# Kernel tuning notes

Measured on AMD Instinct MI355X. Metric: run time of the kernel, lower is better.

Reference implementation:

```python
import jax, jax.numpy as jnp
import numpy as np

TEMPERATURE = 8.0  # sqrt(d_k=64)

def setup_inputs() -> dict:
    key = jax.random.key(0)
    ks = jax.random.split(key, 6)
    shape = (16, 2048, 64)  # [batch*heads, seq_len, d_k]
    names = ["q_real", "k_real", "v_real", "q_phase", "k_phase", "v_phase"]
    return {n: jax.random.normal(k, shape, dtype=jnp.float32) for n, k in zip(names, ks)}

def reference(q_real, k_real, v_real, q_phase, k_phase, v_phase):
    # Complex QK^T scores: (q_r + i q_p)(k_r + i k_p)^H-style split used by the module
    attn_real = jnp.einsum('bqd,bkd->bqk', q_real, k_real) - jnp.einsum('bqd,bkd->bqk', q_phase, k_phase)
    attn_phase = jnp.einsum('bqd,bkd->bqk', q_real, k_phase) + jnp.einsum('bqd,bkd->bqk', q_phase, k_real)
    # continue_complex=True path, mask=None, dropout in eval (p effectively 0)
    attn_real = jax.nn.softmax(attn_real / TEMPERATURE, axis=2)
    attn_phase = jax.nn.softmax(attn_phase / TEMPERATURE, axis=2)
    output_real = jnp.einsum('bqk,bkd->bqd', attn_real, v_real) - jnp.einsum('bqk,bkd->bqd', attn_phase, v_phase)
    output_phase = jnp.einsum('bqk,bkd->bqd', attn_real, v_phase) + jnp.einsum('bqk,bkd->bqd', attn_phase, v_real)
    return output_real, output_phase, attn_real
```

## Files before the change

kernel.cpp:

```cpp
#include <hip/hip_runtime.h>
#include <hip/hip_bf16.h>
#include <stdint.h>

#define BATCH 16
#define SEQ   2048
#define DK    64
#define BQ    (BATCH * SEQ)
#define MAT   ((size_t)BQ * DK)

typedef float  f32x4  __attribute__((ext_vector_type(4)));
typedef __bf16 bf16x8 __attribute__((ext_vector_type(8)));
typedef unsigned short u16x8 __attribute__((ext_vector_type(8)));
typedef unsigned short u16x4 __attribute__((ext_vector_type(4)));

#define MFMA16(a, b, c) __builtin_amdgcn_mfma_f32_16x16x32_bf16((a), (b), (c), 0, 0, 0)

#define TILEU 16384

__device__ __forceinline__ unsigned short bfbits(float f) {
  return __builtin_bit_cast(unsigned short, __float2bfloat16(f));
}

__device__ __forceinline__ void cvt_store(unsigned short* dst, f32x4 a, f32x4 c) {
  u16x8 v;
  v[0] = bfbits(a[0]); v[1] = bfbits(a[1]); v[2] = bfbits(a[2]); v[3] = bfbits(a[3]);
  v[4] = bfbits(c[0]); v[5] = bfbits(c[1]); v[6] = bfbits(c[2]); v[7] = bfbits(c[3]);
  *(u16x8*)dst = v;
}

__device__ __forceinline__ void gload16(const unsigned short* g, unsigned short* l) {
  __builtin_amdgcn_global_load_lds(
      (const __attribute__((address_space(1))) void*)g,
      (__attribute__((address_space(3))) void*)l, 16, 0, 0);
}

__global__ __launch_bounds__(256)
void ck_prep(const float* __restrict__ kr, const float* __restrict__ kp,
             const float* __restrict__ vr, const float* __restrict__ vp,
             const float* __restrict__ qr, const float* __restrict__ qp,
             unsigned short* __restrict__ kv, unsigned short* __restrict__ qb)
{
  __shared__ __align__(16) unsigned short VL[8192];
  const int tid = threadIdx.x;

  if (blockIdx.x >= BATCH * 32) {
    const size_t i8 = ((size_t)(blockIdx.x - BATCH * 32) * 256 + tid) * 8;
    const float* src = (i8 < MAT) ? qr : qp;
    const size_t off = (i8 < MAT) ? i8 : i8 - MAT;
    f32x4 a = *(const f32x4*)(src + off);
    f32x4 c = *(const f32x4*)(src + off + 4);
    cvt_store(qb + i8, a, c);
    return;
  }

  const int b = blockIdx.x >> 5, tile = blockIdx.x & 31;
  unsigned short* blk = kv + (size_t)(b * 32 + tile) * TILEU;
  const size_t go = ((size_t)b * SEQ + tile * 64) * DK;

  {
    const int row = tid >> 2, cp = tid & 3, sw = row & 7;
    const int c0 = cp * 2, c1 = cp * 2 + 1;
    const float* gr = kr + go + (size_t)row * DK + cp * 16;
    f32x4 r0 = ((const f32x4*)gr)[0], r1 = ((const f32x4*)gr)[1];
    f32x4 r2 = ((const f32x4*)gr)[2], r3 = ((const f32x4*)gr)[3];
    const float* gp = kp + go + (size_t)row * DK + cp * 16;
    f32x4 p0 = ((const f32x4*)gp)[0], p1 = ((const f32x4*)gp)[1];
    f32x4 p2 = ((const f32x4*)gp)[2], p3 = ((const f32x4*)gp)[3];
    cvt_store(blk + row * 64 + (c0 ^ sw) * 8, r0, r1);
    cvt_store(blk + row * 64 + (c1 ^ sw) * 8, r2, r3);
    cvt_store(blk + 4096 + row * 64 + (c0 ^ sw) * 8, p0, p1);
    cvt_store(blk + 4096 + row * 64 + (c1 ^ sw) * 8, p2, p3);
  }
  {
    const int key = tid & 15, d0 = (tid >> 4) * 4;
    #pragma unroll
    for (int pass = 0; pass < 4; ++pass) {
      const int kk = pass * 16 + key;
      f32x4 a = *(const f32x4*)(vr + go + (size_t)kk * DK + d0);
      f32x4 c = *(const f32x4*)(vp + go + (size_t)kk * DK + d0);
      const int kc = kk >> 3, kl = kk & 7;
      #pragma unroll
      for (int j = 0; j < 4; ++j) {
        const int d = d0 + j;
        VL[d * 64 + (kc ^ (d & 7)) * 8 + kl]        = bfbits(a[j]);
        VL[4096 + d * 64 + (kc ^ (d & 7)) * 8 + kl] = bfbits(c[j]);
      }
    }
  }
  __syncthreads();
  #pragma unroll
  for (int it = 0; it < 4; ++it)
    *(u16x8*)(blk + 8192 + it * 2048 + tid * 8) = *(const u16x8*)(VL + it * 2048 + tid * 8);
}

__global__ __launch_bounds__(256, 4)
void ck_sums(const unsigned short* __restrict__ qb,
             const unsigned short* __restrict__ kv, float* __restrict__ wsums)
{
  __shared__ __align__(16) unsigned short KT[2][8192];

  const int tid  = threadIdx.x;
  const int wq   = tid >> 6, lane = tid & 63;
  const int lrow = lane & 15, lgrp = lane >> 4;

  const int hw = blockIdx.x;
  const int logical = (hw & 7) * 256 + (hw >> 3);
  const int b = logical >> 7, qtile = (logical >> 2) & 31, slice = logical & 3;

  const int qrow = qtile * 64 + wq * 16 + lrow;
  const size_t qoff = ((size_t)b * SEQ + qrow) * DK;
  bf16x8 aQ0 = __builtin_bit_cast(bf16x8, *(const u16x8*)(qb + qoff + lgrp * 8));
  bf16x8 aQ1 = __builtin_bit_cast(bf16x8, *(const u16x8*)(qb + qoff + 32 + lgrp * 8));
  bf16x8 aQ2 = __builtin_bit_cast(bf16x8, *(const u16x8*)(qb + MAT + qoff + lgrp * 8));
  bf16x8 aQ3 = __builtin_bit_cast(bf16x8, *(const u16x8*)(qb + MAT + qoff + 32 + lgrp * 8));

  auto issue = [&](int tile, int buf) {
    const unsigned short* src = kv + (size_t)(b * 32 + tile) * TILEU;
    #pragma unroll
    for (int c = 0; c < 4; ++c) {
      const int ch = wq * 4 + c;
      gload16(src + ch * 512 + lane * 8, &KT[buf][ch * 512]);
    }
  };

  float lsR[4] = {0.f, 0.f, 0.f, 0.f};
  float lsP[4] = {0.f, 0.f, 0.f, 0.f};

  issue(slice * 8 + 0, 0);
  issue(slice * 8 + 1, 1);
  int cur = 0;
  for (int i = 0; i < 8; ++i) {
    if (i < 7) { asm volatile("s_waitcnt vmcnt(4)" ::: "memory"); }
    else       { asm volatile("s_waitcnt vmcnt(0)" ::: "memory"); }
    __builtin_amdgcn_sched_barrier(0);
    __syncthreads();

    const unsigned short* KB = KT[cur];
    #pragma unroll
    for (int t = 0; t < 4; ++t) {
      const int key16 = t * 16 + lrow;
      const int swk = lrow & 7;
      bf16x8 b0 = __builtin_bit_cast(bf16x8, *(const u16x8*)&KB[key16 * 64 + ((lgrp    ) ^ swk) * 8]);
      bf16x8 b1 = __builtin_bit_cast(bf16x8, *(const u16x8*)&KB[key16 * 64 + ((lgrp + 4) ^ swk) * 8]);
      bf16x8 b2 = __builtin_bit_cast(bf16x8, *(const u16x8*)&KB[4096 + key16 * 64 + ((lgrp    ) ^ swk) * 8]);
      bf16x8 b3 = __builtin_bit_cast(bf16x8, *(const u16x8*)&KB[4096 + key16 * 64 + ((lgrp + 4) ^ swk) * 8]);
      f32x4 t1 = {}, t2 = {}, sp = {};
      t1 = MFMA16(aQ0, b0, t1); t1 = MFMA16(aQ1, b1, t1);
      t2 = MFMA16(aQ2, b2, t2); t2 = MFMA16(aQ3, b3, t2);
      sp = MFMA16(aQ0, b2, sp); sp = MFMA16(aQ1, b3, sp);
      sp = MFMA16(aQ2, b0, sp); sp = MFMA16(aQ3, b1, sp);
      #pragma unroll
      for (int r = 0; r < 4; ++r) {
        lsR[r] += __expf((t1[r] - t2[r]) * 0.125f);
        lsP[r] += __expf(sp[r] * 0.125f);
      }
    }
    __syncthreads();
    if (i + 2 < 8) issue(slice * 8 + i + 2, cur);
    cur ^= 1;
  }

  #pragma unroll
  for (int r = 0; r < 4; ++r) {
    float sR = lsR[r], sP = lsP[r];
    #pragma unroll
    for (int m = 1; m < 16; m <<= 1) {
      sR += __shfl_xor(sR, m, 64);
      sP += __shfl_xor(sP, m, 64);
    }
    if (lrow == 0) {
      const size_t row = (size_t)b * SEQ + qtile * 64 + wq * 16 + lgrp * 4 + r;
      wsums[(size_t)(slice * 2 + 0) * BQ + row] = sR;
      wsums[(size_t)(slice * 2 + 1) * BQ + row] = sP;
    }
  }
}

__global__ __launch_bounds__(256, 2)
void ck_main(const unsigned short* __restrict__ qb,
             const unsigned short* __restrict__ kv,
             const float* __restrict__ wsums, float* __restrict__ dout)
{
  __shared__ __align__(16) unsigned short KV[2][16384];
  __shared__ __align__(16) unsigned short Pr[64][32], Pp[64][32];

  const int tid  = threadIdx.x;
  const int wq   = tid >> 6, lane = tid & 63;
  const int lrow = lane & 15, lgrp = lane >> 4;

  const int hw = blockIdx.x;
  const int logical = (hw & 7) * 64 + (hw >> 3);
  const int b = logical >> 5, qtile = logical & 31;

  float* outR = dout;
  float* outP = dout + MAT;
  float* attn = dout + 2 * MAT + ((size_t)b * SEQ + (size_t)qtile * 64) * SEQ;

  const int qrow = qtile * 64 + wq * 16 + lrow;
  const size_t qoff = ((size_t)b * SEQ + qrow) * DK;
  bf16x8 aQ0 = __builtin_bit_cast(bf16x8, *(const u16x8*)(qb + qoff + lgrp * 8));
  bf16x8 aQ1 = __builtin_bit_cast(bf16x8, *(const u16x8*)(qb + qoff + 32 + lgrp * 8));
  bf16x8 aQ2 = __builtin_bit_cast(bf16x8, *(const u16x8*)(qb + MAT + qoff + lgrp * 8));
  bf16x8 aQ3 = __builtin_bit_cast(bf16x8, *(const u16x8*)(qb + MAT + qoff + 32 + lgrp * 8));

  const int qloc = wq * 16 + lgrp * 4;
  float iR[4], iP[4];
  {
    const size_t base = (size_t)b * SEQ + qtile * 64 + qloc;
    #pragma unroll
    for (int r = 0; r < 4; ++r) {
      float sR = 0.f, sP = 0.f;
      #pragma unroll
      for (int z = 0; z < 4; ++z) {
        sR += wsums[(size_t)(z * 2 + 0) * BQ + base + r];
        sP += wsums[(size_t)(z * 2 + 1) * BQ + base + r];
      }
      iR[r] = 1.0f / sR;
      iP[r] = 1.0f / sP;
    }
  }

  auto issue = [&](int tile, int buf) {
    const unsigned short* src = kv + (size_t)(b * 32 + tile) * TILEU;
    #pragma unroll
    for (int c = 0; c < 8; ++c) {
      const int ch = wq * 8 + c;
      gload16(src + ch * 512 + lane * 8, &KV[buf][ch * 512]);
    }
  };

  const u16x8 SGN = {0x8000, 0x8000, 0x8000, 0x8000, 0x8000, 0x8000, 0x8000, 0x8000};
  f32x4 accR[4] = {}, accP[4] = {};

  issue(0, 0);
  issue(1, 1);
  int cur = 0;
  for (int i = 0; i < 32; ++i) {
    const int k0 = i * 64;
    if (i < 31) { asm volatile("s_waitcnt vmcnt(8)" ::: "memory"); }
    else        { asm volatile("s_waitcnt vmcnt(0)" ::: "memory"); }
    __builtin_amdgcn_sched_barrier(0);
    __syncthreads();

    const unsigned short* KB = KV[cur];
    #pragma unroll
    for (int h = 0; h < 2; ++h) {
      #pragma unroll
      for (int t = 0; t < 2; ++t) {
        const int key16 = (h * 2 + t) * 16 + lrow;
        const int swk = lrow & 7;
        bf16x8 b0 = __builtin_bit_cast(bf16x8, *(const u16x8*)&KB[key16 * 64 + ((lgrp    ) ^ swk) * 8]);
        bf16x8 b1 = __builtin_bit_cast(bf16x8, *(const u16x8*)&KB[key16 * 64 + ((lgrp + 4) ^ swk) * 8]);
        bf16x8 b2 = __builtin_bit_cast(bf16x8, *(const u16x8*)&KB[4096 + key16 * 64 + ((lgrp    ) ^ swk) * 8]);
        bf16x8 b3 = __builtin_bit_cast(bf16x8, *(const u16x8*)&KB[4096 + key16 * 64 + ((lgrp + 4) ^ swk) * 8]);
        f32x4 t1 = {}, t2 = {}, sp = {};
        t1 = MFMA16(aQ0, b0, t1); t1 = MFMA16(aQ1, b1, t1);
        t2 = MFMA16(aQ2, b2, t2); t2 = MFMA16(aQ3, b3, t2);
        sp = MFMA16(aQ0, b2, sp); sp = MFMA16(aQ1, b3, sp);
        sp = MFMA16(aQ2, b0, sp); sp = MFMA16(aQ3, b1, sp);
        #pragma unroll
        for (int r = 0; r < 4; ++r) {
          const float er = __expf((t1[r] - t2[r]) * 0.125f) * iR[r];
          const float ep = __expf(sp[r] * 0.125f) * iP[r];
          const int row = qloc + r, col = t * 16 + lrow;
          const int pc = ((col >> 3) ^ (row & 3)) * 8 + (col & 7);
          Pr[row][pc] = bfbits(er);
          Pp[row][pc] = bfbits(ep);
        }
      }
      {
        const int prow = wq * 16 + lrow;
        u16x8 uar = *(const u16x8*)&Pr[prow][(lgrp ^ (prow & 3)) * 8];
        u16x8 uap = *(const u16x8*)&Pp[prow][(lgrp ^ (prow & 3)) * 8];
        u16x8 uan = uap ^ SGN;
        bf16x8 apr = __builtin_bit_cast(bf16x8, uar);
        bf16x8 app = __builtin_bit_cast(bf16x8, uap);
        bf16x8 apn = __builtin_bit_cast(bf16x8, uan);
        #pragma unroll
        for (int nt = 0; nt < 4; ++nt) {
          const int d = nt * 16 + lrow;
          const int cv = ((h * 4 + lgrp) ^ (d & 7)) * 8;
          bf16x8 bvr = __builtin_bit_cast(bf16x8, *(const u16x8*)&KB[8192  + d * 64 + cv]);
          bf16x8 bvp = __builtin_bit_cast(bf16x8, *(const u16x8*)&KB[12288 + d * 64 + cv]);
          accR[nt] = MFMA16(apr, bvr, accR[nt]);
          accR[nt] = MFMA16(apn, bvp, accR[nt]);
          accP[nt] = MFMA16(apr, bvp, accP[nt]);
          accP[nt] = MFMA16(app, bvr, accP[nt]);
        }
      }
      {
        const int j8 = lane & 7;
        #pragma unroll
        for (int s = 0; s < 2; ++s) {
          const int arow = wq * 16 + s * 8 + (lane >> 3);
          const int pc = (((j8 >> 1) ^ (arow & 3)) * 8) + (j8 & 1) * 4;
          u16x4 ua = *(const u16x4*)&Pr[arow][pc];
          f32x4 fa;
          #pragma unroll
          for (int q = 0; q < 4; ++q)
            fa[q] = __builtin_bit_cast(float, (unsigned)ua[q] << 16);
          float* dst = attn + (size_t)arow * SEQ + k0 + h * 32 + j8 * 4;
          __builtin_nontemporal_store(fa, (f32x4*)dst);
        }
      }
    }
    __syncthreads();
    if (i + 2 < 32) issue(i + 2, cur);
    cur ^= 1;
  }

  #pragma unroll
  for (int nt = 0; nt < 4; ++nt) {
    const int d = nt * 16 + lrow;
    #pragma unroll
    for (int r = 0; r < 4; ++r) {
      const size_t o = ((size_t)b * SEQ + qtile * 64 + qloc + r) * DK + d;
      outR[o] = accR[nt][r];
      outP[o] = accP[nt][r];
    }
  }
}

extern "C" void kernel_launch(void* const* d_in, const int* in_sizes, int n_in,
                              void* d_out, int out_size, void* d_ws, size_t ws_size,
                              hipStream_t stream)
{
  const float* qr = (const float*)d_in[0];
  const float* kr = (const float*)d_in[1];
  const float* vr = (const float*)d_in[2];
  const float* qp = (const float*)d_in[3];
  const float* kp = (const float*)d_in[4];
  const float* vp = (const float*)d_in[5];
  float* out = (float*)d_out;

  unsigned short* kv = (unsigned short*)d_ws;
  unsigned short* qb = (unsigned short*)((char*)d_ws + (16u << 20));
  float* wsums = (float*)((char*)d_ws + (24u << 20));

  const unsigned qblocks = (unsigned)(2 * MAT / 8 / 256);
  ck_prep<<<BATCH * 32 + qblocks, 256, 0, stream>>>(kr, kp, vr, vp, qr, qp, kv, qb);
  ck_sums<<<4 * 32 * BATCH, 256, 0, stream>>>(qb, kv, wsums);
  ck_main<<<32 * BATCH, 256, 0, stream>>>(qb, kv, wsums, out);
}
```

Baseline: 149.9 us.

## Process two query tiles per block in row-sum kernel and relax load waits

The softmax denominator kernel now computes two 64-row query tiles per block, reusing each staged K tile for twice the MFMA work and halving the grid. This cuts redundant K tile loads into LDS. The main kernel's vmcnt wait thresholds are raised, apparently to discount outstanding attention stores so the wait does not also stall on writes. The risk is higher register pressure and fewer blocks in the sums kernel, plus correctness depending on the store count assumption.

New measurement: 163.7 us. +9.2%, slower.

```diff
diff --git a/kernel.cpp b/kernel.cpp
--- a/kernel.cpp
+++ b/kernel.cpp
@@ -26,6 +26,10 @@
   v[0] = bfbits(a[0]); v[1] = bfbits(a[1]); v[2] = bfbits(a[2]); v[3] = bfbits(a[3]);
   v[4] = bfbits(c[0]); v[5] = bfbits(c[1]); v[6] = bfbits(c[2]); v[7] = bfbits(c[3]);
   *(u16x8*)dst = v;
+}
+
+__device__ __forceinline__ bf16x8 ldbf(const unsigned short* p) {
+  return __builtin_bit_cast(bf16x8, *(const u16x8*)p);
 }
 
 __device__ __forceinline__ void gload16(const unsigned short* g, unsigned short* l) {
@@ -104,15 +108,23 @@
   const int lrow = lane & 15, lgrp = lane >> 4;
 
   const int hw = blockIdx.x;
-  const int logical = (hw & 7) * 256 + (hw >> 3);
-  const int b = logical >> 7, qtile = (logical >> 2) & 31, slice = logical & 3;
-
-  const int qrow = qtile * 64 + wq * 16 + lrow;
-  const size_t qoff = ((size_t)b * SEQ + qrow) * DK;
-  bf16x8 aQ0 = __builtin_bit_cast(bf16x8, *(const u16x8*)(qb + qoff + lgrp * 8));
-  bf16x8 aQ1 = __builtin_bit_cast(bf16x8, *(const u16x8*)(qb + qoff + 32 + lgrp * 8));
-  bf16x8 aQ2 = __builtin_bit_cast(bf16x8, *(const u16x8*)(qb + MAT + qoff + lgrp * 8));
-  bf16x8 aQ3 = __builtin_bit_cast(bf16x8, *(const u16x8*)(qb + MAT + qoff + 32 + lgrp * 8));
+  const int logical = (hw & 7) * 128 + (hw >> 3);
+  const int b = logical >> 6, qpair = (logical >> 2) & 15, slice = logical & 3;
+
+  bf16x8 aQ[8];
+  {
+    const int qrowA = qpair * 128 + wq * 16 + lrow;
+    const size_t qoffA = ((size_t)b * SEQ + qrowA) * DK;
+    const size_t qoffB = qoffA + (size_t)64 * DK;
+    aQ[0] = ldbf(qb + qoffA + lgrp * 8);
+    aQ[1] = ldbf(qb + qoffA + 32 + lgrp * 8);
+    aQ[2] = ldbf(qb + MAT + qoffA + lgrp * 8);
+    aQ[3] = ldbf(qb + MAT + qoffA + 32 + lgrp * 8);
+    aQ[4] = ldbf(qb + qoffB + lgrp * 8);
+    aQ[5] = ldbf(qb + qoffB + 32 + lgrp * 8);
+    aQ[6] = ldbf(qb + MAT + qoffB + lgrp * 8);
+    aQ[7] = ldbf(qb + MAT + qoffB + 32 + lgrp * 8);
+  }
 
   auto issue = [&](int tile, int buf) {
     const unsigned short* src = kv + (size_t)(b * 32 + tile) * TILEU;
@@ -123,8 +135,8 @@
     }
   };
 
-  float lsR[4] = {0.f, 0.f, 0.f, 0.f};
-  float lsP[4] = {0.f, 0.f, 0.f, 0.f};
+  float lsR[2][4] = {};
+  float lsP[2][4] = {};
 
   issue(slice * 8 + 0, 0);
   issue(slice * 8 + 1, 1);
@@ -140,19 +152,22 @@
     for (int t = 0; t < 4; ++t) {
       const int key16 = t * 16 + lrow;
       const int swk = lrow & 7;
-      bf16x8 b0 = __builtin_bit_cast(bf16x8, *(const u16x8*)&KB[key16 * 64 + ((lgrp    ) ^ swk) * 8]);
-      bf16x8 b1 = __builtin_bit_cast(bf16x8, *(const u16x8*)&KB[key16 * 64 + ((lgrp + 4) ^ swk) * 8]);
-      bf16x8 b2 = __builtin_bit_cast(bf16x8, *(const u16x8*)&KB[4096 + key16 * 64 + ((lgrp    ) ^ swk) * 8]);
-      bf16x8 b3 = __builtin_bit_cast(bf16x8, *(const u16x8*)&KB[4096 + key16 * 64 + ((lgrp + 4) ^ swk) * 8]);
-      f32x4 t1 = {}, t2 = {}, sp = {};
-      t1 = MFMA16(aQ0, b0, t1); t1 = MFMA16(aQ1, b1, t1);
-      t2 = MFMA16(aQ2, b2, t2); t2 = MFMA16(aQ3, b3, t2);
-      sp = MFMA16(aQ0, b2, sp); sp = MFMA16(aQ1, b3, sp);
-      sp = MFMA16(aQ2, b0, sp); sp = MFMA16(aQ3, b1, sp);
-      #pragma unroll
-      for (int r = 0; r < 4; ++r) {
-        lsR[r] += __expf((t1[r] - t2[r]) * 0.125f);
-        lsP[r] += __expf(sp[r] * 0.125f);
+      bf16x8 b0 = ldbf(&KB[key16 * 64 + ((lgrp    ) ^ swk) * 8]);
+      bf16x8 b1 = ldbf(&KB[key16 * 64 + ((lgrp + 4) ^ swk) * 8]);
+      bf16x8 b2 = ldbf(&KB[4096 + key16 * 64 + ((lgrp    ) ^ swk) * 8]);
+      bf16x8 b3 = ldbf(&KB[4096 + key16 * 64 + ((lgrp + 4) ^ swk) * 8]);
+      #pragma unroll
+      for (int g = 0; g < 2; ++g) {
+        f32x4 t1 = {}, t2 = {}, sp = {};
+        t1 = MFMA16(aQ[g * 4 + 0], b0, t1); t1 = MFMA16(aQ[g * 4 + 1], b1, t1);
+        t2 = MFMA16(aQ[g * 4 + 2], b2, t2); t2 = MFMA16(aQ[g * 4 + 3], b3, t2);
+        sp = MFMA16(aQ[g * 4 + 0], b2, sp); sp = MFMA16(aQ[g * 4 + 1], b3, sp);
+        sp = MFMA16(aQ[g * 4 + 2], b0, sp); sp = MFMA16(aQ[g * 4 + 3], b1, sp);
+        #pragma unroll
+        for (int r = 0; r < 4; ++r) {
+          lsR[g][r] += __expf((t1[r] - t2[r]) * 0.125f);
+          lsP[g][r] += __expf(sp[r] * 0.125f);
+        }
       }
     }
     __syncthreads();
@@ -161,17 +176,20 @@
   }
 
   #pragma unroll
-  for (int r = 0; r < 4; ++r) {
-    float sR = lsR[r], sP = lsP[r];
-    #pragma unroll
-    for (int m = 1; m < 16; m <<= 1) {
-      sR += __shfl_xor(sR, m, 64);
-      sP += __shfl_xor(sP, m, 64);
-    }
-    if (lrow == 0) {
-      const size_t row = (size_t)b * SEQ + qtile * 64 + wq * 16 + lgrp * 4 + r;
-      wsums[(size_t)(slice * 2 + 0) * BQ + row] = sR;
-      wsums[(size_t)(slice * 2 + 1) * BQ + row] = sP;
+  for (int g = 0; g < 2; ++g) {
+    #pragma unroll
+    for (int r = 0; r < 4; ++r) {
+      float sR = lsR[g][r], sP = lsP[g][r];
+      #pragma unroll
+      for (int m = 1; m < 16; m <<= 1) {
+        sR += __shfl_xor(sR, m, 64);
+        sP += __shfl_xor(sP, m, 64);
+      }
+      if (lrow == 0) {
+        const size_t row = (size_t)b * SEQ + qpair * 128 + g * 64 + wq * 16 + lgrp * 4 + r;
+        wsums[(size_t)(slice * 2 + 0) * BQ + row] = sR;
+        wsums[(size_t)(slice * 2 + 1) * BQ + row] = sP;
+      }
     }
   }
 }
@@ -198,10 +216,10 @@
 
   const int qrow = qtile * 64 + wq * 16 + lrow;
   const size_t qoff = ((size_t)b * SEQ + qrow) * DK;
-  bf16x8 aQ0 = __builtin_bit_cast(bf16x8, *(const u16x8*)(qb + qoff + lgrp * 8));
-  bf16x8 aQ1 = __builtin_bit_cast(bf16x8, *(const u16x8*)(qb + qoff + 32 + lgrp * 8));
-  bf16x8 aQ2 = __builtin_bit_cast(bf16x8, *(const u16x8*)(qb + MAT + qoff + lgrp * 8));
-  bf16x8 aQ3 = __builtin_bit_cast(bf16x8, *(const u16x8*)(qb + MAT + qoff + 32 + lgrp * 8));
+  bf16x8 aQ0 = ldbf(qb + qoff + lgrp * 8);
+  bf16x8 aQ1 = ldbf(qb + qoff + 32 + lgrp * 8);
+  bf16x8 aQ2 = ldbf(qb + MAT + qoff + lgrp * 8);
+  bf16x8 aQ3 = ldbf(qb + MAT + qoff + 32 + lgrp * 8);
 
   const int qloc = wq * 16 + lgrp * 4;
   float iR[4], iP[4];
@@ -237,8 +255,9 @@
   int cur = 0;
   for (int i = 0; i < 32; ++i) {
     const int k0 = i * 64;
-    if (i < 31) { asm volatile("s_waitcnt vmcnt(8)" ::: "memory"); }
-    else        { asm volatile("s_waitcnt vmcnt(0)" ::: "memory"); }
+    if (i == 0)      { asm volatile("s_waitcnt vmcnt(8)"  ::: "memory"); }
+    else if (i < 31) { asm volatile("s_waitcnt vmcnt(12)" ::: "memory"); }
+    else             { asm volatile("s_waitcnt vmcnt(4)"  ::: "memory"); }
     __builtin_amdgcn_sched_barrier(0);
     __syncthreads();
 
@@ -249,10 +268,10 @@
       for (int t = 0; t < 2; ++t) {
         const int key16 = (h * 2 + t) * 16 + lrow;
         const int swk = lrow & 7;
-        bf16x8 b0 = __builtin_bit_cast(bf16x8, *(const u16x8*)&KB[key16 * 64 + ((lgrp    ) ^ swk) * 8]);
-        bf16x8 b1 = __builtin_bit_cast(bf16x8, *(const u16x8*)&KB[key16 * 64 + ((lgrp + 4) ^ swk) * 8]);
-        bf16x8 b2 = __builtin_bit_cast(bf16x8, *(const u16x8*)&KB[4096 + key16 * 64 + ((lgrp    ) ^ swk) * 8]);
-        bf16x8 b3 = __builtin_bit_cast(bf16x8, *(const u16x8*)&KB[4096 + key16 * 64 + ((lgrp + 4) ^ swk) * 8]);
+        bf16x8 b0 = ldbf(&KB[key16 * 64 + ((lgrp    ) ^ swk) * 8]);
+        bf16x8 b1 = ldbf(&KB[key16 * 64 + ((lgrp + 4) ^ swk) * 8]);
+        bf16x8 b2 = ldbf(&KB[4096 + key16 * 64 + ((lgrp    ) ^ swk) * 8]);
+        bf16x8 b3 = ldbf(&KB[4096 + key16 * 64 + ((lgrp + 4) ^ swk) * 8]);
         f32x4 t1 = {}, t2 = {}, sp = {};
         t1 = MFMA16(aQ0, b0, t1); t1 = MFMA16(aQ1, b1, t1);
         t2 = MFMA16(aQ2, b2, t2); t2 = MFMA16(aQ3, b3, t2);
@@ -280,8 +299,8 @@
         for (int nt = 0; nt < 4; ++nt) {
           const int d = nt * 16 + lrow;
           const int cv = ((h * 4 + lgrp) ^ (d & 7)) * 8;
-          bf16x8 bvr = __builtin_bit_cast(bf16x8, *(const u16x8*)&KB[8192  + d * 64 + cv]);
-          bf16x8 bvp = __builtin_bit_cast(bf16x8, *(const u16x8*)&KB[12288 + d * 64 + cv]);
+          bf16x8 bvr = ldbf(&KB[8192  + d * 64 + cv]);
+          bf16x8 bvp = ldbf(&KB[12288 + d * 64 + cv]);
           accR[nt] = MFMA16(apr, bvr, accR[nt]);
           accR[nt] = MFMA16(apn, bvp, accR[nt]);
           accP[nt] = MFMA16(apr, bvp, accP[nt]);
@@ -339,6 +358,6 @@
 
   const unsigned qblocks = (unsigned)(2 * MAT / 8 / 256);
   ck_prep<<<BATCH * 32 + qblocks, 256, 0, stream>>>(kr, kp, vr, vp, qr, qp, kv, qb);
-  ck_sums<<<4 * 32 * BATCH, 256, 0, stream>>>(qb, kv, wsums);
+  ck_sums<<<2 * 32 * BATCH, 256, 0, stream>>>(qb, kv, wsums);
   ck_main<<<32 * BATCH, 256, 0, stream>>>(qb, kv, wsums, out);
 }
```
